# Optimization experiments

Measured on AMD Instinct MI355X. Metric: run time of the kernel, lower is better.

Reference implementation:

```python
import jax, jax.numpy as jnp
import numpy as np

N_NODES = 100000
N_EDGES = 1600000
DROP_P = 0.5  # F.dropout default, training=True by default in the source
LRELU_SLOPE = 0.01
EPS = 1e-12


def setup_inputs() -> dict:
    key = jax.random.key(0)
    ks = jax.random.split(key, 8)
    x = jax.random.normal(ks[0], (N_NODES, 64), dtype=jnp.float32)
    edge_index = jax.random.randint(ks[1], (2, N_EDGES), 0, N_NODES, dtype=jnp.int64)
    s = 1.0 / np.sqrt(64)
    W1_l = jax.random.uniform(ks[2], (64, 32), jnp.float32, -s, s)
    W1_r = jax.random.uniform(ks[3], (64, 32), jnp.float32, -s, s)
    b1 = jnp.zeros((32,), jnp.float32)
    s2 = 1.0 / np.sqrt(32)
    W2_l = jax.random.uniform(ks[4], (32, 64), jnp.float32, -s2, s2)
    W2_r = jax.random.uniform(ks[5], (32, 64), jnp.float32, -s2, s2)
    b2 = jnp.zeros((64,), jnp.float32)
    return {"x": x, "edge_index": edge_index, "W1_l": W1_l, "b1": b1,
            "W1_r": W1_r, "W2_l": W2_l, "b2": b2, "W2_r": W2_r}


def _sage_conv(x, src, dst, W_l, b, W_r, n):
    # mean aggregation of source features onto destinations (PyG SAGEConv)
    msg = x[src]                                                 # [E, d]
    agg = jax.ops.segment_sum(msg, dst, num_segments=n)          # [N, d]
    cnt = jax.ops.segment_sum(jnp.ones((src.shape[0],), x.dtype), dst, num_segments=n)
    mean = agg / jnp.maximum(cnt, 1.0)[:, None]
    return mean @ W_l + b + x @ W_r


def _dropout(x, key):
    keep = jax.random.bernoulli(key, 1.0 - DROP_P, x.shape)
    return jnp.where(keep, x / (1.0 - DROP_P), 0.0).astype(x.dtype)


def reference(x, edge_index, W1_l, b1, W1_r, W2_l, b2, W2_r):
    n = x.shape[0]
    src, dst = edge_index[0], edge_index[1]
    dk = jax.random.split(jax.random.key(42), 2)
    h = _sage_conv(x, src, dst, W1_l, b1, W1_r, n)
    h = jax.nn.leaky_relu(h, LRELU_SLOPE)
    h = _dropout(h, dk[0])
    h = _sage_conv(h, src, dst, W2_l, b2, W2_r, n)
    h = _dropout(h, dk[1])
    norm = jnp.sqrt(jnp.sum(h * h, axis=1, keepdims=True))
    return h / jnp.maximum(norm, EPS)
```

## Files before the change

### kernel.cpp

```cpp
#include <hip/hip_runtime.h>

#define N_NODES 100000
#define N_EDGES 1600000
#define NPB 32
#define NB (N_NODES / NPB)
#define CAP 704
#define NCC 49
#define CAPA 34816
#define NFB 64
#define BPC 16
#define N16 (N_NODES * 16)
#define GHB 6250

typedef float v2f __attribute__((ext_vector_type(2)));

struct U2 { unsigned a, b; };

__host__ __device__ constexpr U2 tf2x32(unsigned k0, unsigned k1, unsigned c0, unsigned c1) {
  unsigned ks2 = k0 ^ k1 ^ 0x1BD11BDAu;
  unsigned x0 = c0 + k0, x1 = c1 + k1;
#define TFR(r) { x0 += x1; x1 = (x1 << (r)) | (x1 >> (32 - (r))); x1 ^= x0; }
  TFR(13) TFR(15) TFR(26) TFR(6)
  x0 += k1;  x1 += ks2 + 1u;
  TFR(17) TFR(29) TFR(16) TFR(24)
  x0 += ks2; x1 += k0 + 2u;
  TFR(13) TFR(15) TFR(26) TFR(6)
  x0 += k0;  x1 += k1 + 3u;
  TFR(17) TFR(29) TFR(16) TFR(24)
  x0 += k1;  x1 += ks2 + 4u;
  TFR(13) TFR(15) TFR(26) TFR(6)
  x0 += ks2; x1 += k0 + 5u;
#undef TFR
  return U2{x0, x1};
}

constexpr U2 DK0 = tf2x32(0u, 42u, 0u, 0u);
constexpr U2 DK1 = tf2x32(0u, 42u, 0u, 1u);

__device__ __forceinline__ bool keep_bit(unsigned k0, unsigned k1, unsigned j) {
  U2 w = tf2x32(k0, k1, 0u, j);
  return ((w.a ^ w.b) >> 31) == 0u;
}

__device__ __forceinline__ unsigned short f2bf(float f) {
  unsigned u = __float_as_uint(f);
  u += 0x7FFFu + ((u >> 16) & 1u);
  return (unsigned short)(u >> 16);
}
__device__ __forceinline__ v2f up2(unsigned r) {
  v2f v;
  v.x = __uint_as_float(r << 16);
  v.y = __uint_as_float(r & 0xFFFF0000u);
  return v;
}

__global__ __launch_bounds__(256, 4) void k_transform1(
    const float* __restrict__ x, const float* __restrict__ Wl,
    const float* __restrict__ Wr, unsigned short* __restrict__ xlbh,
    float* __restrict__ xr) {
  __shared__ __align__(16) float rv[4][64];
  int lane = threadIdx.x & 63;
  int wv = (threadIdx.x >> 6) & 3;
  const float* W = (lane < 32) ? Wl : Wr;
  int c = lane & 31;
  float w[64];
#pragma unroll
  for (int k = 0; k < 64; ++k) w[k] = W[k * 32 + c];
  int wid0 = (int)((blockIdx.x * blockDim.x + threadIdx.x) >> 6);
  int wstride = (int)((gridDim.x * blockDim.x) >> 6);
  for (int wid = wid0; wid < N_NODES; wid += wstride) {
    float xv = x[wid * 64 + lane];
    asm volatile("s_waitcnt lgkmcnt(0)" ::: "memory");
    rv[wv][lane] = xv;
    asm volatile("s_waitcnt lgkmcnt(0)" ::: "memory");
    v2f s0 = {0.f, 0.f}, s1 = {0.f, 0.f};
#pragma unroll
    for (int k = 0; k < 64; k += 4) {
      float4 r = *(const float4*)&rv[wv][k];
      v2f w0; w0.x = w[k + 0]; w0.y = w[k + 1];
      v2f w1; w1.x = w[k + 2]; w1.y = w[k + 3];
      v2f p0; p0.x = r.x; p0.y = r.y;
      v2f p1; p1.x = r.z; p1.y = r.w;
      s0 += p0 * w0;
      s1 += p1 * w1;
    }
    float s = (s0.x + s0.y) + (s1.x + s1.y);
    if (lane < 32) xlbh[(size_t)(c >> 4) * N16 + wid * 16 + (c & 15)] = f2bf(s);
    else           xr[wid * 32 + c] = s;
  }
}

__global__ __launch_bounds__(256) void k_binA(
    const int* __restrict__ src, const int* __restrict__ dst,
    int* __restrict__ curA, unsigned* __restrict__ bufA) {
  __shared__ int hist[NCC];
  __shared__ int offsL[NCC + 1];
  __shared__ int baseL[NCC];
  __shared__ int place[NCC];
  __shared__ unsigned stag[2048];
  __shared__ unsigned char cellb[2048];
  int t = threadIdx.x;
  for (long long start = (long long)blockIdx.x * 2048; start < N_EDGES;
       start += (long long)gridDim.x * 2048) {
    int n = (int)min((long long)2048, (long long)N_EDGES - start);
    for (int i = t; i < NCC; i += 256) hist[i] = 0;
    __syncthreads();
    unsigned pv[8]; int pc[8];
#pragma unroll
    for (int i = 0; i < 8; ++i) {
      int idx = t + i * 256;
      if (idx < n) {
        int d = dst[start + idx];
        int s = src[start + idx];
        int cc = d >> 11;
        pc[i] = cc;
        pv[i] = (unsigned)s | ((unsigned)(d & 2047) << 17);
        atomicAdd(&hist[cc], 1);
      } else pc[i] = -1;
    }
    __syncthreads();
    if (t < 64) {
      int lane = t;
      int v = (lane < NCC) ? hist[lane] : 0;
      int x = v;
#pragma unroll
      for (int o = 1; o < 64; o <<= 1) {
        int y = __shfl_up(x, o, 64);
        if (lane >= o) x += y;
      }
      if (lane < NCC) {
        offsL[lane] = x - v;
        place[lane] = 0;
        if (v > 0) baseL[lane] = atomicAdd(&curA[lane], v);
      }
      if (lane == NCC - 1) offsL[NCC] = x;
    }
    __syncthreads();
#pragma unroll
    for (int i = 0; i < 8; ++i) {
      if (pc[i] >= 0) {
        int p = atomicAdd(&place[pc[i]], 1);
        int sl = offsL[pc[i]] + p;
        stag[sl] = pv[i];
        cellb[sl] = (unsigned char)pc[i];
      }
    }
    __syncthreads();
    for (int s2 = t; s2 < n; s2 += 256) {
      int cell = cellb[s2];
      int pos = baseL[cell] + (s2 - offsL[cell]);
      if (pos < CAPA) bufA[(size_t)cell * CAPA + pos] = stag[s2];
    }
    __syncthreads();
  }
}

__global__ __launch_bounds__(256) void k_binB(
    const unsigned* __restrict__ bufA, const int* __restrict__ curA,
    int* __restrict__ cur, unsigned* __restrict__ buf) {
  __shared__ int hist[NFB];
  __shared__ int offsL[NFB + 1];
  __shared__ int baseL[NFB];
  __shared__ int place[NFB];
  __shared__ unsigned stag[2048];
  __shared__ unsigned char cellb[2048];
  int cellc = blockIdx.x / BPC;
  int slice = blockIdx.x % BPC;
  int t = threadIdx.x;
  int cnt = min(curA[cellc], CAPA);
  const unsigned* in = bufA + (size_t)cellc * CAPA;
  for (int start = slice * 2048; start < cnt; start += BPC * 2048) {
    int n = min(2048, cnt - start);
    for (int i = t; i < NFB; i += 256) hist[i] = 0;
    __syncthreads();
    unsigned pv[8]; int pb[8];
#pragma unroll
    for (int i = 0; i < 8; ++i) {
      int idx = t + i * 256;
      if (idx < n) {
        unsigned w = in[start + idx];
        int dlow = (int)(w >> 17);
        int fb = dlow >> 5;
        pb[i] = fb;
        pv[i] = (w & 0x1FFFFu) | ((unsigned)(dlow & 31) << 17);
        atomicAdd(&hist[fb], 1);
      } else pb[i] = -1;
    }
    __syncthreads();
    if (t < 64) {
      int lane = t;
      int v = hist[lane];
      int x = v;
#pragma unroll
      for (int o = 1; o < 64; o <<= 1) {
        int y = __shfl_up(x, o, 64);
        if (lane >= o) x += y;
      }
      offsL[lane] = x - v;
      place[lane] = 0;
      if (v > 0) baseL[lane] = atomicAdd(&cur[cellc * NFB + lane], v);
      if (lane == 63) offsL[NFB] = x;
    }
    __syncthreads();
#pragma unroll
    for (int i = 0; i < 8; ++i) {
      if (pb[i] >= 0) {
        int p = atomicAdd(&place[pb[i]], 1);
        int sl = offsL[pb[i]] + p;
        stag[sl] = pv[i];
        cellb[sl] = (unsigned char)pb[i];
      }
    }
    __syncthreads();
    for (int s2 = t; s2 < n; s2 += 256) {
      int fb = cellb[s2];
      int pos = baseL[fb] + (s2 - offsL[fb]);
      if (pos < CAP) buf[(size_t)(cellc * NFB + fb) * CAP + pos] = stag[s2];
    }
    __syncthreads();
  }
}

__global__ __launch_bounds__(1024) void k_bscan(
    const int* __restrict__ cur, int* __restrict__ bbase) {
  __shared__ int warp_sums[16];
  __shared__ int s_running;
  int t = threadIdx.x;
  int lane = t & 63, w = t >> 6;
  if (t == 0) s_running = 0;
  __syncthreads();
  for (int base = 0; base < NB; base += 1024) {
    int i = base + t;
    int v = (i < NB) ? min(cur[i], CAP) : 0;
    int x = v;
#pragma unroll
    for (int o = 1; o < 64; o <<= 1) {
      int y = __shfl_up(x, o, 64);
      if (lane >= o) x += y;
    }
    if (lane == 63) warp_sums[w] = x;
    __syncthreads();
    if (w == 0) {
      int ws = (lane < 16) ? warp_sums[lane] : 0;
#pragma unroll
      for (int o = 1; o < 16; o <<= 1) {
        int y = __shfl_up(ws, o, 64);
        if (lane >= o) ws += y;
      }
      if (lane < 16) warp_sums[lane] = ws;
    }
    __syncthreads();
    int incl = x + (w > 0 ? warp_sums[w - 1] : 0);
    int excl = s_running + incl - v;
    if (i < NB) bbase[i] = excl;
    __syncthreads();
    if (t == 1023) s_running += incl;
    __syncthreads();
  }
}

__global__ __launch_bounds__(256) void k_bfill(
    const unsigned* __restrict__ buf, const int* __restrict__ cur,
    const int* __restrict__ bbase, int* __restrict__ deg,
    int* __restrict__ offs, int* __restrict__ eidx) {
  __shared__ int ncnt[NPB];
  __shared__ int ncur[NPB];
  __shared__ unsigned sbuf[CAP];
  int b = blockIdx.x, t = threadIdx.x;
  if (t < NPB) ncnt[t] = 0;
  __syncthreads();
  int nb = min(cur[b], CAP);
  const unsigned* bb = buf + (size_t)b * CAP;
  for (int slot = t; slot < nb; slot += 256) {
    unsigned w = bb[slot];
    sbuf[slot] = w;
    atomicAdd(&ncnt[w >> 17], 1);
  }
  __syncthreads();
  if (t < 64) {
    int lane = t;
    int c = (lane < NPB) ? ncnt[lane] : 0;
    int x = c;
#pragma unroll
    for (int o = 1; o < 32; o <<= 1) {
      int y = __shfl_up(x, o, 64);
      if (lane >= o) x += y;
    }
    if (lane < NPB) {
      int excl = x - c;
      ncur[lane] = excl;
      int gn = b * NPB + lane;
      deg[gn] = c;
      offs[gn] = bbase[b] + excl;
    }
  }
  __syncthreads();
  int base = bbase[b];
  for (int slot = t; slot < nb; slot += 256) {
    unsigned w = sbuf[slot];
    int p = atomicAdd(&ncur[w >> 17], 1);
    eidx[base + p] = (int)(w & 0x1FFFF);
  }
}

__global__ __launch_bounds__(256) void k_gather1(
    const unsigned short* __restrict__ xlbh, const float* __restrict__ xr,
    const int* __restrict__ offs, const int* __restrict__ deg,
    const int* __restrict__ eidx, const float* __restrict__ b1,
    unsigned short* __restrict__ hpbh) {
  int bb = blockIdx.x;
  int G = 0, nb = bb;
  if (nb >= GHB) { G = 1; nb -= GHB; }
  int tid = threadIdx.x;
  int lane = tid & 63;
  int node = nb * 16 + (tid >> 4);
  int g = (tid >> 2) & 3;
  int ch = tid & 3;
  int c = tid & 15;
  int col = G * 16 + c;
  int off = offs[node];
  int dg = deg[node];
  float xr_v = xr[node * 32 + col];
  float b1_v = b1[col];
  const uint2* H = (const uint2*)(xlbh + (size_t)G * N16);
  v2f acc01 = {0.f, 0.f}, acc23 = {0.f, 0.f};
  int k = 0;
  for (; k + 8 <= dg; k += 8) {
    int s0 = eidx[off + k + g];
    int s1 = eidx[off + k + 4 + g];
    uint2 r0 = H[s0 * 4 + ch];
    uint2 r1 = H[s1 * 4 + ch];
    acc01 += up2(r0.x); acc23 += up2(r0.y);
    acc01 += up2(r1.x); acc23 += up2(r1.y);
  }
  for (; k < dg; k += 4) {
    if (k + g < dg) {
      int s = eidx[off + k + g];
      uint2 r = H[s * 4 + ch];
      acc01 += up2(r.x); acc23 += up2(r.y);
    }
  }
  float a0 = acc01.x, a1 = acc01.y, a2 = acc23.x, a3 = acc23.y;
  a0 += __shfl_xor(a0, 4, 64); a0 += __shfl_xor(a0, 8, 64);
  a1 += __shfl_xor(a1, 4, 64); a1 += __shfl_xor(a1, 8, 64);
  a2 += __shfl_xor(a2, 4, 64); a2 += __shfl_xor(a2, 8, 64);
  a3 += __shfl_xor(a3, 4, 64); a3 += __shfl_xor(a3, 8, 64);
  int srcl = (lane & 48) + (c >> 2);
  float t0 = __shfl(a0, srcl, 64);
  float t1 = __shfl(a1, srcl, 64);
  float t2 = __shfl(a2, srcl, 64);
  float t3 = __shfl(a3, srcl, 64);
  int sub = lane & 3;
  float val = (sub == 0) ? t0 : (sub == 1) ? t1 : (sub == 2) ? t2 : t3;
  float inv = 1.0f / fmaxf((float)dg, 1.0f);
  int j = node * 32 + col;
  float v = val * inv + b1_v + xr_v;
  v = (v > 0.f) ? v : 0.01f * v;
  float h = keep_bit(DK0.a, DK0.b, (unsigned)j) ? 2.0f * v : 0.0f;
  hpbh[(size_t)G * N16 + node * 16 + c] = f2bf(h);
}

__global__ __launch_bounds__(256) void k_gather2(
    const unsigned short* __restrict__ hpbh, const int* __restrict__ offs,
    const int* __restrict__ deg, const int* __restrict__ eidx,
    float* __restrict__ aggh) {
  int bb = blockIdx.x;
  int G = 0, nb = bb;
  if (nb >= GHB) { G = 1; nb -= GHB; }
  int tid = threadIdx.x;
  int lane = tid & 63;
  int node = nb * 16 + (tid >> 4);
  int g = (tid >> 2) & 3;
  int ch = tid & 3;
  int c = tid & 15;
  int off = offs[node];
  int dg = deg[node];
  const uint2* H = (const uint2*)(hpbh + (size_t)G * N16);
  v2f acc01 = {0.f, 0.f}, acc23 = {0.f, 0.f};
  int k = 0;
  for (; k + 8 <= dg; k += 8) {
    int s0 = eidx[off + k + g];
    int s1 = eidx[off + k + 4 + g];
    uint2 r0 = H[s0 * 4 + ch];
    uint2 r1 = H[s1 * 4 + ch];
    acc01 += up2(r0.x); acc23 += up2(r0.y);
    acc01 += up2(r1.x); acc23 += up2(r1.y);
  }
  for (; k < dg; k += 4) {
    if (k + g < dg) {
      int s = eidx[off + k + g];
      uint2 r = H[s * 4 + ch];
      acc01 += up2(r.x); acc23 += up2(r.y);
    }
  }
  float a0 = acc01.x, a1 = acc01.y, a2 = acc23.x, a3 = acc23.y;
  a0 += __shfl_xor(a0, 4, 64); a0 += __shfl_xor(a0, 8, 64);
  a1 += __shfl_xor(a1, 4, 64); a1 += __shfl_xor(a1, 8, 64);
  a2 += __shfl_xor(a2, 4, 64); a2 += __shfl_xor(a2, 8, 64);
  a3 += __shfl_xor(a3, 4, 64); a3 += __shfl_xor(a3, 8, 64);
  int srcl = (lane & 48) + (c >> 2);
  float t0 = __shfl(a0, srcl, 64);
  float t1 = __shfl(a1, srcl, 64);
  float t2 = __shfl(a2, srcl, 64);
  float t3 = __shfl(a3, srcl, 64);
  int sub = lane & 3;
  float val = (sub == 0) ? t0 : (sub == 1) ? t1 : (sub == 2) ? t2 : t3;
  float inv = 1.0f / fmaxf((float)dg, 1.0f);
  aggh[(size_t)G * N16 + node * 16 + c] = val * inv;
}

__global__ __launch_bounds__(256, 4) void k_out2(
    const unsigned short* __restrict__ hpbh, const float* __restrict__ aggh,
    const float* __restrict__ W2l, const float* __restrict__ b2,
    const float* __restrict__ W2r, float* __restrict__ out) {
  __shared__ __align__(16) float rv[4][64];
  int lane = threadIdx.x & 63;
  int wv = (threadIdx.x >> 6) & 3;
  float wl[32], wr[32];
#pragma unroll
  for (int kk = 0; kk < 32; ++kk) {
    wl[kk] = W2l[kk * 64 + lane];
    wr[kk] = W2r[kk * 64 + lane];
  }
  float bias = b2[lane];
  int wid0 = (int)((blockIdx.x * blockDim.x + threadIdx.x) >> 6);
  int wstride = (int)((gridDim.x * blockDim.x) >> 6);
  for (int wid = wid0; wid < N_NODES; wid += wstride) {
    asm volatile("s_waitcnt lgkmcnt(0)" ::: "memory");
    if (lane < 8) {
      const float* ap = aggh + ((lane < 4) ? 0 : (size_t)N16) + wid * 16 + (lane & 3) * 4;
      float4 v = *(const float4*)ap;
      *(float4*)&rv[wv][lane * 4] = v;
    } else if (lane < 16) {
      const uint2* Hp = (const uint2*)(hpbh + ((lane < 12) ? 0 : (size_t)N16));
      uint2 o = Hp[wid * 4 + (lane & 3)];
      float4 v;
      v.x = __uint_as_float(o.x << 16);
      v.y = __uint_as_float(o.x & 0xFFFF0000u);
      v.z = __uint_as_float(o.y << 16);
      v.w = __uint_as_float(o.y & 0xFFFF0000u);
      *(float4*)&rv[wv][32 + (lane - 8) * 4] = v;
    }
    asm volatile("s_waitcnt lgkmcnt(0)" ::: "memory");
    v2f sa = {0.f, 0.f}, sb = {0.f, 0.f};
#pragma unroll
    for (int kk = 0; kk < 32; kk += 4) {
      float4 r1 = *(const float4*)&rv[wv][kk];
      float4 r2 = *(const float4*)&rv[wv][32 + kk];
      v2f w0; w0.x = wl[kk + 0]; w0.y = wl[kk + 1];
      v2f w1; w1.x = wl[kk + 2]; w1.y = wl[kk + 3];
      v2f u0; u0.x = wr[kk + 0]; u0.y = wr[kk + 1];
      v2f u1; u1.x = wr[kk + 2]; u1.y = wr[kk + 3];
      v2f p0; p0.x = r1.x; p0.y = r1.y;
      v2f p1; p1.x = r1.z; p1.y = r1.w;
      v2f q0; q0.x = r2.x; q0.y = r2.y;
      v2f q1; q1.x = r2.z; q1.y = r2.w;
      sa += p0 * w0;  sa += p1 * w1;
      sb += q0 * u0;  sb += q1 * u1;
    }
    float v = (sa.x + sa.y) + (sb.x + sb.y) + bias;
    unsigned j = (unsigned)(wid * 64 + lane);
    float d = keep_bit(DK1.a, DK1.b, j) ? 2.0f * v : 0.0f;
    float ss = d * d;
#pragma unroll
    for (int o = 32; o > 0; o >>= 1) ss += __shfl_xor(ss, o, 64);
    float scale = 1.0f / fmaxf(sqrtf(ss), 1e-12f);
    out[j] = d * scale;
  }
}

extern "C" void kernel_launch(void* const* d_in, const int* in_sizes, int n_in,
                              void* d_out, int out_size, void* d_ws, size_t ws_size,
                              hipStream_t stream) {
  const float* x   = (const float*)d_in[0];
  const int*   ei  = (const int*)d_in[1];
  const float* W1l = (const float*)d_in[2];
  const float* b1  = (const float*)d_in[3];
  const float* W1r = (const float*)d_in[4];
  const float* W2l = (const float*)d_in[5];
  const float* b2  = (const float*)d_in[6];
  const float* W2r = (const float*)d_in[7];
  float* out = (float*)d_out;

  const int* src = ei;
  const int* dst = ei + N_EDGES;

  const size_t F32 = (size_t)N_NODES * 32;
  char* w = (char*)d_ws;
  unsigned* bufA = (unsigned*)w;
  float* xr      = (float*)w;
  float* aggh    = (float*)w;
  w += F32 * sizeof(float);
  unsigned* buf  = (unsigned*)w;
  unsigned short* xlbh = (unsigned short*)w;
  unsigned short* hpbh = xlbh + 2 * (size_t)N16;
  w += F32 * 2 * sizeof(unsigned short);
  int* curA  = (int*)w; w += NCC * sizeof(int);
  int* cur   = (int*)w; w += NB * sizeof(int);
  int* bbase = (int*)w; w += NB * sizeof(int);
  int* deg   = (int*)w; w += N_NODES * sizeof(int);
  int* offs  = (int*)w; w += N_NODES * sizeof(int);
  int* eidx  = (int*)w;

  hipMemsetAsync(curA, 0, (size_t)(NCC + NB) * sizeof(int), stream);

  k_binA<<<(N_EDGES + 2047) / 2048, 256, 0, stream>>>(src, dst, curA, bufA);
  k_binB<<<NCC * BPC, 256, 0, stream>>>(bufA, curA, cur, buf);
  k_bscan<<<1, 1024, 0, stream>>>(cur, bbase);
  k_bfill<<<NB, 256, 0, stream>>>(buf, cur, bbase, deg, offs, eidx);

  k_transform1<<<1024, 256, 0, stream>>>(x, W1l, W1r, xlbh, xr);
  k_gather1<<<2 * GHB, 256, 0, stream>>>(xlbh, xr, offs, deg, eidx, b1, hpbh);
  k_gather2<<<2 * GHB, 256, 0, stream>>>(hpbh, offs, deg, eidx, aggh);
  k_out2<<<1024, 256, 0, stream>>>(hpbh, aggh, W2l, b2, W2r, out);
}
```

Before: 272.9 us.

## Precompute dropout masks in a separate kernel and prefetch rows in dense kernels

Adds a k_mask kernel that evaluates the threefry dropout bits for both layers once and packs them into 64-bit ballot words. The gather1 and out2 kernels now read a mask word instead of running the hash inline. The transform1 and out2 kernels double-buffer their LDS row staging and prefetch the next node's inputs to overlap global loads with the FMAs. Weights are held in float4 registers, and the grid grows from 1024 to 1280 blocks. This adds an extra launch and extra mask memory traffic in exchange for moving the hash work off the critical kernels.

```diff
diff --git a/kernel.cpp b/kernel.cpp
--- a/kernel.cpp
+++ b/kernel.cpp
@@ -11,6 +11,8 @@
 #define BPC 16
 #define N16 (N_NODES * 16)
 #define GHB 6250
+#define M1W 50000
+#define M2W 100000
 
 typedef float v2f __attribute__((ext_vector_type(2)));
 
@@ -54,39 +56,73 @@
   return v;
 }
 
+__device__ __forceinline__ float4 ldcol(const float* __restrict__ W, int i,
+                                        int lane, int ld) {
+  float4 v;
+  v.x = W[(i * 4 + 0) * ld + lane];
+  v.y = W[(i * 4 + 1) * ld + lane];
+  v.z = W[(i * 4 + 2) * ld + lane];
+  v.w = W[(i * 4 + 3) * ld + lane];
+  return v;
+}
+
+__global__ __launch_bounds__(256) void k_mask(unsigned long long* __restrict__ msk) {
+  int w = (int)((blockIdx.x * blockDim.x + threadIdx.x) >> 6);
+  int lane = threadIdx.x & 63;
+  int nw = (int)((gridDim.x * blockDim.x) >> 6);
+  for (; w < M1W + M2W; w += nw) {
+    unsigned k0, k1, j;
+    if (w < M1W) { k0 = DK0.a; k1 = DK0.b; j = (unsigned)w * 64u + (unsigned)lane; }
+    else { k0 = DK1.a; k1 = DK1.b; j = (unsigned)(w - M1W) * 64u + (unsigned)lane; }
+    unsigned long long bits = __ballot(keep_bit(k0, k1, j));
+    if (lane == 0) msk[w] = bits;
+  }
+}
+
 __global__ __launch_bounds__(256, 4) void k_transform1(
     const float* __restrict__ x, const float* __restrict__ Wl,
     const float* __restrict__ Wr, unsigned short* __restrict__ xlbh,
     float* __restrict__ xr) {
-  __shared__ __align__(16) float rv[4][64];
+  __shared__ __align__(16) float rv[2][4][64];
   int lane = threadIdx.x & 63;
   int wv = (threadIdx.x >> 6) & 3;
   const float* W = (lane < 32) ? Wl : Wr;
   int c = lane & 31;
-  float w[64];
-#pragma unroll
-  for (int k = 0; k < 64; ++k) w[k] = W[k * 32 + c];
+  float4 V0 = ldcol(W, 0, c, 32),  V1 = ldcol(W, 1, c, 32);
+  float4 V2 = ldcol(W, 2, c, 32),  V3 = ldcol(W, 3, c, 32);
+  float4 V4 = ldcol(W, 4, c, 32),  V5 = ldcol(W, 5, c, 32);
+  float4 V6 = ldcol(W, 6, c, 32),  V7 = ldcol(W, 7, c, 32);
+  float4 V8 = ldcol(W, 8, c, 32),  V9 = ldcol(W, 9, c, 32);
+  float4 V10 = ldcol(W, 10, c, 32), V11 = ldcol(W, 11, c, 32);
+  float4 V12 = ldcol(W, 12, c, 32), V13 = ldcol(W, 13, c, 32);
+  float4 V14 = ldcol(W, 14, c, 32), V15 = ldcol(W, 15, c, 32);
   int wid0 = (int)((blockIdx.x * blockDim.x + threadIdx.x) >> 6);
   int wstride = (int)((gridDim.x * blockDim.x) >> 6);
+  float xv = x[wid0 * 64 + lane];
+  int b = 0;
   for (int wid = wid0; wid < N_NODES; wid += wstride) {
-    float xv = x[wid * 64 + lane];
+    rv[b][wv][lane] = xv;
+    int nxt = wid + wstride;
+    if (nxt < N_NODES) xv = x[nxt * 64 + lane];
     asm volatile("s_waitcnt lgkmcnt(0)" ::: "memory");
-    rv[wv][lane] = xv;
-    asm volatile("s_waitcnt lgkmcnt(0)" ::: "memory");
+    const float* rb = &rv[b][wv][0];
     v2f s0 = {0.f, 0.f}, s1 = {0.f, 0.f};
-#pragma unroll
-    for (int k = 0; k < 64; k += 4) {
-      float4 r = *(const float4*)&rv[wv][k];
-      v2f w0; w0.x = w[k + 0]; w0.y = w[k + 1];
-      v2f w1; w1.x = w[k + 2]; w1.y = w[k + 3];
-      v2f p0; p0.x = r.x; p0.y = r.y;
-      v2f p1; p1.x = r.z; p1.y = r.w;
-      s0 += p0 * w0;
-      s1 += p1 * w1;
-    }
+#define TST(Vi, i) { \
+    float4 r = *(const float4*)(rb + (i) * 4); \
+    v2f w0; w0.x = Vi.x; w0.y = Vi.y; \
+    v2f w1; w1.x = Vi.z; w1.y = Vi.w; \
+    v2f p0; p0.x = r.x; p0.y = r.y; \
+    v2f p1; p1.x = r.z; p1.y = r.w; \
+    s0 += p0 * w0; s1 += p1 * w1; }
+    TST(V0, 0)  TST(V1, 1)  TST(V2, 2)  TST(V3, 3)
+    TST(V4, 4)  TST(V5, 5)  TST(V6, 6)  TST(V7, 7)
+    TST(V8, 8)  TST(V9, 9)  TST(V10, 10) TST(V11, 11)
+    TST(V12, 12) TST(V13, 13) TST(V14, 14) TST(V15, 15)
+#undef TST
     float s = (s0.x + s0.y) + (s1.x + s1.y);
     if (lane < 32) xlbh[(size_t)(c >> 4) * N16 + wid * 16 + (c & 15)] = f2bf(s);
     else           xr[wid * 32 + c] = s;
+    b ^= 1;
   }
 }
 
@@ -307,6 +343,7 @@
     const unsigned short* __restrict__ xlbh, const float* __restrict__ xr,
     const int* __restrict__ offs, const int* __restrict__ deg,
     const int* __restrict__ eidx, const float* __restrict__ b1,
+    const unsigned long long* __restrict__ msk1,
     unsigned short* __restrict__ hpbh) {
   int bb = blockIdx.x;
   int G = 0, nb = bb;
@@ -322,6 +359,8 @@
   int dg = deg[node];
   float xr_v = xr[node * 32 + col];
   float b1_v = b1[col];
+  unsigned jj = (unsigned)(node * 32 + col);
+  unsigned long long mw = msk1[jj >> 6];
   const uint2* H = (const uint2*)(xlbh + (size_t)G * N16);
   v2f acc01 = {0.f, 0.f}, acc23 = {0.f, 0.f};
   int k = 0;
@@ -353,10 +392,9 @@
   int sub = lane & 3;
   float val = (sub == 0) ? t0 : (sub == 1) ? t1 : (sub == 2) ? t2 : t3;
   float inv = 1.0f / fmaxf((float)dg, 1.0f);
-  int j = node * 32 + col;
   float v = val * inv + b1_v + xr_v;
   v = (v > 0.f) ? v : 0.01f * v;
-  float h = keep_bit(DK0.a, DK0.b, (unsigned)j) ? 2.0f * v : 0.0f;
+  float h = ((mw >> (jj & 63)) & 1ull) ? 2.0f * v : 0.0f;
   hpbh[(size_t)G * N16 + node * 16 + c] = f2bf(h);
 }
 
@@ -412,61 +450,73 @@
 __global__ __launch_bounds__(256, 4) void k_out2(
     const unsigned short* __restrict__ hpbh, const float* __restrict__ aggh,
     const float* __restrict__ W2l, const float* __restrict__ b2,
-    const float* __restrict__ W2r, float* __restrict__ out) {
-  __shared__ __align__(16) float rv[4][64];
+    const float* __restrict__ W2r, const unsigned long long* __restrict__ msk2,
+    float* __restrict__ out) {
+  __shared__ __align__(16) float rv[2][4][64];
   int lane = threadIdx.x & 63;
   int wv = (threadIdx.x >> 6) & 3;
-  float wl[32], wr[32];
-#pragma unroll
-  for (int kk = 0; kk < 32; ++kk) {
-    wl[kk] = W2l[kk * 64 + lane];
-    wr[kk] = W2r[kk * 64 + lane];
-  }
+  float4 L0 = ldcol(W2l, 0, lane, 64), L1 = ldcol(W2l, 1, lane, 64);
+  float4 L2 = ldcol(W2l, 2, lane, 64), L3 = ldcol(W2l, 3, lane, 64);
+  float4 L4 = ldcol(W2l, 4, lane, 64), L5 = ldcol(W2l, 5, lane, 64);
+  float4 L6 = ldcol(W2l, 6, lane, 64), L7 = ldcol(W2l, 7, lane, 64);
+  float4 R0 = ldcol(W2r, 0, lane, 64), R1 = ldcol(W2r, 1, lane, 64);
+  float4 R2 = ldcol(W2r, 2, lane, 64), R3 = ldcol(W2r, 3, lane, 64);
+  float4 R4 = ldcol(W2r, 4, lane, 64), R5 = ldcol(W2r, 5, lane, 64);
+  float4 R6 = ldcol(W2r, 6, lane, 64), R7 = ldcol(W2r, 7, lane, 64);
   float bias = b2[lane];
   int wid0 = (int)((blockIdx.x * blockDim.x + threadIdx.x) >> 6);
   int wstride = (int)((gridDim.x * blockDim.x) >> 6);
+  float4 pa; uint2 ph;
+#define PRELOAD(widx) { \
+  if (lane < 8) { \
+    const float* ap = aggh + ((lane < 4) ? 0 : (size_t)N16) + (size_t)(widx) * 16 + (lane & 3) * 4; \
+    pa = *(const float4*)ap; \
+  } else if (lane < 16) { \
+    const uint2* Hp = (const uint2*)(hpbh + ((lane < 12) ? 0 : (size_t)N16)); \
+    ph = Hp[(size_t)(widx) * 4 + (lane & 3)]; \
+  } }
+  PRELOAD(wid0);
+  int b = 0;
   for (int wid = wid0; wid < N_NODES; wid += wstride) {
+    if (lane < 8) {
+      *(float4*)&rv[b][wv][lane * 4] = pa;
+    } else if (lane < 16) {
+      v2f lo = up2(ph.x), hi = up2(ph.y);
+      float4 v; v.x = lo.x; v.y = lo.y; v.z = hi.x; v.w = hi.y;
+      *(float4*)&rv[b][wv][32 + (lane - 8) * 4] = v;
+    }
+    int nxt = wid + wstride;
+    if (nxt < N_NODES) PRELOAD(nxt);
+    unsigned long long mw = msk2[wid];
     asm volatile("s_waitcnt lgkmcnt(0)" ::: "memory");
-    if (lane < 8) {
-      const float* ap = aggh + ((lane < 4) ? 0 : (size_t)N16) + wid * 16 + (lane & 3) * 4;
-      float4 v = *(const float4*)ap;
-      *(float4*)&rv[wv][lane * 4] = v;
-    } else if (lane < 16) {
-      const uint2* Hp = (const uint2*)(hpbh + ((lane < 12) ? 0 : (size_t)N16));
-      uint2 o = Hp[wid * 4 + (lane & 3)];
-      float4 v;
-      v.x = __uint_as_float(o.x << 16);
-      v.y = __uint_as_float(o.x & 0xFFFF0000u);
-      v.z = __uint_as_float(o.y << 16);
-      v.w = __uint_as_float(o.y & 0xFFFF0000u);
-      *(float4*)&rv[wv][32 + (lane - 8) * 4] = v;
-    }
-    asm volatile("s_waitcnt lgkmcnt(0)" ::: "memory");
+    const float* rb = &rv[b][wv][0];
     v2f sa = {0.f, 0.f}, sb = {0.f, 0.f};
-#pragma unroll
-    for (int kk = 0; kk < 32; kk += 4) {
-      float4 r1 = *(const float4*)&rv[wv][kk];
-      float4 r2 = *(const float4*)&rv[wv][32 + kk];
-      v2f w0; w0.x = wl[kk + 0]; w0.y = wl[kk + 1];
-      v2f w1; w1.x = wl[kk + 2]; w1.y = wl[kk + 3];
-      v2f u0; u0.x = wr[kk + 0]; u0.y = wr[kk + 1];
-      v2f u1; u1.x = wr[kk + 2]; u1.y = wr[kk + 3];
-      v2f p0; p0.x = r1.x; p0.y = r1.y;
-      v2f p1; p1.x = r1.z; p1.y = r1.w;
-      v2f q0; q0.x = r2.x; q0.y = r2.y;
-      v2f q1; q1.x = r2.z; q1.y = r2.w;
-      sa += p0 * w0;  sa += p1 * w1;
-      sb += q0 * u0;  sb += q1 * u1;
-    }
+#define GST(Li, Ri, i) { \
+    float4 r1 = *(const float4*)(rb + (i) * 4); \
+    float4 r2 = *(const float4*)(rb + 32 + (i) * 4); \
+    v2f w0; w0.x = Li.x; w0.y = Li.y; \
+    v2f w1; w1.x = Li.z; w1.y = Li.w; \
+    v2f u0; u0.x = Ri.x; u0.y = Ri.y; \
+    v2f u1; u1.x = Ri.z; u1.y = Ri.w; \
+    v2f p0; p0.x = r1.x; p0.y = r1.y; \
+    v2f p1; p1.x = r1.z; p1.y = r1.w; \
+    v2f q0; q0.x = r2.x; q0.y = r2.y; \
+    v2f q1; q1.x = r2.z; q1.y = r2.w; \
+    sa += p0 * w0; sa += p1 * w1; \
+    sb += q0 * u0; sb += q1 * u1; }
+    GST(L0, R0, 0) GST(L1, R1, 1) GST(L2, R2, 2) GST(L3, R3, 3)
+    GST(L4, R4, 4) GST(L5, R5, 5) GST(L6, R6, 6) GST(L7, R7, 7)
+#undef GST
     float v = (sa.x + sa.y) + (sb.x + sb.y) + bias;
-    unsigned j = (unsigned)(wid * 64 + lane);
-    float d = keep_bit(DK1.a, DK1.b, j) ? 2.0f * v : 0.0f;
+    float d = ((mw >> lane) & 1ull) ? 2.0f * v : 0.0f;
     float ss = d * d;
 #pragma unroll
     for (int o = 32; o > 0; o >>= 1) ss += __shfl_xor(ss, o, 64);
     float scale = 1.0f / fmaxf(sqrtf(ss), 1e-12f);
-    out[j] = d * scale;
-  }
+    out[(size_t)wid * 64 + lane] = d * scale;
+    b ^= 1;
+  }
+#undef PRELOAD
 }
 
 extern "C" void kernel_launch(void* const* d_in, const int* in_sizes, int n_in,
@@ -500,17 +550,19 @@
   int* bbase = (int*)w; w += NB * sizeof(int);
   int* deg   = (int*)w; w += N_NODES * sizeof(int);
   int* offs  = (int*)w; w += N_NODES * sizeof(int);
-  int* eidx  = (int*)w;
+  int* eidx  = (int*)w; w += (size_t)N_EDGES * sizeof(int);
+  unsigned long long* msk = (unsigned long long*)w;
 
   hipMemsetAsync(curA, 0, (size_t)(NCC + NB) * sizeof(int), stream);
 
+  k_mask<<<2048, 256, 0, stream>>>(msk);
   k_binA<<<(N_EDGES + 2047) / 2048, 256, 0, stream>>>(src, dst, curA, bufA);
   k_binB<<<NCC * BPC, 256, 0, stream>>>(bufA, curA, cur, buf);
   k_bscan<<<1, 1024, 0, stream>>>(cur, bbase);
   k_bfill<<<NB, 256, 0, stream>>>(buf, cur, bbase, deg, offs, eidx);
 
-  k_transform1<<<1024, 256, 0, stream>>>(x, W1l, W1r, xlbh, xr);
-  k_gather1<<<2 * GHB, 256, 0, stream>>>(xlbh, xr, offs, deg, eidx, b1, hpbh);
+  k_transform1<<<1280, 256, 0, stream>>>(x, W1l, W1r, xlbh, xr);
+  k_gather1<<<2 * GHB, 256, 0, stream>>>(xlbh, xr, offs, deg, eidx, b1, msk, hpbh);
   k_gather2<<<2 * GHB, 256, 0, stream>>>(hpbh, offs, deg, eidx, aggh);
-  k_out2<<<1024, 256, 0, stream>>>(hpbh, aggh, W2l, b2, W2r, out);
-}
+  k_out2<<<1280, 256, 0, stream>>>(hpbh, aggh, W2l, b2, W2r, msk + M1W, out);
+}
```

Result: slower. 290.3 us (+6.3%).
